# Kernel tuning notes

Measured on AMD Instinct MI355X. Metric: run time of the kernel, lower is better.

Reference implementation:

```python
import jax, jax.numpy as jnp
import numpy as np

B, N, C = 8, 4096, 512

def setup_inputs() -> dict:
    key = jax.random.key(0)
    k1, k2, k3, k4, k5, k6 = jax.random.split(key, 6)
    x = jax.random.normal(k1, (B, N, C), dtype=jnp.float32)
    adj = jax.random.uniform(k2, (B, C, C), dtype=jnp.float32)
    # params: stored [in, out] so y = x @ W + b (equivalent to torch Linear)
    s = 1.0 / np.sqrt(C)
    Wqkv = jax.random.uniform(k3, (C, 3 * C), dtype=jnp.float32, minval=-s, maxval=s)
    bqkv = jax.random.uniform(k4, (3 * C,), dtype=jnp.float32, minval=-s, maxval=s)
    Wo = jax.random.uniform(k5, (C, C), dtype=jnp.float32, minval=-s, maxval=s)
    bo = jax.random.uniform(k6, (C,), dtype=jnp.float32, minval=-s, maxval=s)
    return {"x": x, "adj": adj, "Wqkv": Wqkv, "bqkv": bqkv, "Wo": Wo, "bo": bo}

def reference(x, adj, Wqkv, bqkv, Wo, bo):
    # qkv projection + ReLU gating
    qkv = jnp.einsum('bnc,cd->bnd', x, Wqkv) + bqkv          # [B,N,3C]
    q, k, v = jnp.split(qkv, 3, axis=-1)                      # each [B,N,C]
    q, k, v = jax.nn.relu(q), jax.nn.relu(k), jax.nn.relu(v)
    dk = q.shape[-1]
    # channel-wise scores: q^T k over tokens -> [B,C,C]
    scores = jnp.einsum('bnc,bnd->bcd', q, k) / jnp.sqrt(jnp.float32(dk))
    attn = jax.nn.softmax(scores, axis=-1)
    attn = attn * adj                                         # post-softmax adjacency gate
    y = jnp.einsum('bnc,bcd->bnd', v, attn)                   # value.matmul(attention)
    return jnp.einsum('bnc,cd->bnd', y, Wo) + bo
```

## Files before the change

### kernel.cpp

```cpp
#include <hip/hip_runtime.h>

#define B_ 8
#define N_ 4096
#define C_ 512

typedef _Float16 f16;
typedef __attribute__((ext_vector_type(8))) _Float16 f16x8;
typedef __attribute__((ext_vector_type(4))) _Float16 f16x4;
typedef __attribute__((ext_vector_type(4))) float f32x4;

#define TILE_E (128 * 32)

#define GLL16(gsrc, ldst)                                                      \
  __builtin_amdgcn_global_load_lds(                                            \
      (const __attribute__((address_space(1))) void*)(gsrc),                   \
      (__attribute__((address_space(3))) void*)(ldst), 16, 0, 0)

__device__ __forceinline__ int xcd_remap(int bid, int nwg) {
  return (bid & 7) * (nwg >> 3) + (bid >> 3);
}

#define SBAR() asm volatile("s_barrier" ::: "memory")
#define SFENCE() __builtin_amdgcn_sched_barrier(0)

template <int LDA, int LDB, int NT>
__device__ __forceinline__ void mainloop8(const f16* __restrict__ Ag,
                                          const f16* __restrict__ Bg,
                                          f16* Als, f16* Bls,
                                          f32x4 (&acc)[8][4]) {
  const int tid = threadIdx.x;
  const int lane = tid & 63;
  const int wv = tid >> 6;
  const int wr = wv >> 2;
  const int wcq = wv & 3;

  const int kpart = ((lane >> 4) * 8) ^ ((lane & 4) << 2);
  const int abase = (lane & 15) * 64 + kpart;
  const int bbase = ((wcq & 1) * 64 + (lane & 15)) * 64 + kpart;

  int rowl[2], colb[2];
#pragma unroll
  for (int ld = 0; ld < 2; ++ld) {
    const int doff = (ld * 512 + tid) * 16;
    const int off2 = doff ^ (((doff >> 9) & 1) << 5);
    rowl[ld] = off2 >> 7;
    colb[ld] = off2 & 127;
  }

  const char* Agb = (const char*)Ag;
  const char* Bgb = (const char*)Bg;

  auto stage = [&](int t, int mat, int h) {
    if (t >= NT) return;
    const char* gb = mat ? Bgb : Agb;
    const int ldm2 = (mat ? LDB : LDA) * 2;
    f16* lsl = (mat ? Bls : Als) + ((t & 1) * 2 + h) * 8192 + wv * 512;
#pragma unroll
    for (int ld = 0; ld < 2; ++ld) {
      const char* src =
          gb + (size_t)(h * 128 + rowl[ld]) * ldm2 + (size_t)t * 128 + colb[ld];
      GLL16(src, lsl + ld * 4096);
    }
  };

  stage(0, 0, 0); stage(0, 0, 1); stage(0, 1, 0); stage(0, 1, 1);
  stage(1, 0, 0); stage(1, 0, 1); stage(1, 1, 0);
  asm volatile("s_waitcnt vmcnt(6)" ::: "memory");
  SBAR();
  SFENCE();

  for (int T = 0; T < NT; ++T) {
    const f16* Ab = Als + ((T & 1) * 2 + wr) * 8192;
    const f16* Bb = Bls + ((T & 1) * 2 + (wcq >> 1)) * 8192;
    stage(T + 1, 1, 1);
    f16x8 af[8][2], bf[4][2];
#pragma unroll
    for (int m = 0; m < 8; ++m)
#pragma unroll
      for (int s = 0; s < 2; ++s)
        af[m][s] = *(const f16x8*)(Ab + abase + m * 1024 + s * 32);
#pragma unroll
    for (int n = 0; n < 4; ++n)
#pragma unroll
      for (int s = 0; s < 2; ++s)
        bf[n][s] = *(const f16x8*)(Bb + bbase + n * 1024 + s * 32);
    asm volatile("" ::: "memory");
    SBAR();
    asm volatile("s_waitcnt lgkmcnt(0)" ::: "memory");
    SFENCE();
    __builtin_amdgcn_s_setprio(1);
#pragma unroll
    for (int m = 0; m < 4; ++m)
#pragma unroll
      for (int n = 0; n < 4; ++n)
        acc[m][n] = __builtin_amdgcn_mfma_f32_16x16x32_f16(af[m][0], bf[n][0],
                                                           acc[m][n], 0, 0, 0);
    __builtin_amdgcn_s_setprio(0);
    SBAR();
    SFENCE();
    stage(T + 2, 0, 0);
    SBAR();
    __builtin_amdgcn_s_setprio(1);
#pragma unroll
    for (int m = 4; m < 8; ++m)
#pragma unroll
      for (int n = 0; n < 4; ++n)
        acc[m][n] = __builtin_amdgcn_mfma_f32_16x16x32_f16(af[m][0], bf[n][0],
                                                           acc[m][n], 0, 0, 0);
    __builtin_amdgcn_s_setprio(0);
    SBAR();
    SFENCE();
    stage(T + 2, 0, 1);
    SBAR();
    __builtin_amdgcn_s_setprio(1);
#pragma unroll
    for (int m = 0; m < 4; ++m)
#pragma unroll
      for (int n = 0; n < 4; ++n)
        acc[m][n] = __builtin_amdgcn_mfma_f32_16x16x32_f16(af[m][1], bf[n][1],
                                                           acc[m][n], 0, 0, 0);
    __builtin_amdgcn_s_setprio(0);
    SBAR();
    SFENCE();
    stage(T + 2, 1, 0);
    if (T + 2 < NT) {
      asm volatile("s_waitcnt vmcnt(6)" ::: "memory");
    } else {
      asm volatile("s_waitcnt vmcnt(0)" ::: "memory");
    }
    SBAR();
    __builtin_amdgcn_s_setprio(1);
#pragma unroll
    for (int m = 4; m < 8; ++m)
#pragma unroll
      for (int n = 0; n < 4; ++n)
        acc[m][n] = __builtin_amdgcn_mfma_f32_16x16x32_f16(af[m][1], bf[n][1],
                                                           acc[m][n], 0, 0, 0);
    __builtin_amdgcn_s_setprio(0);
    SBAR();
    SFENCE();
  }
}

#define ZERO_ACC8(acc)                                                         \
  f32x4 acc[8][4];                                                             \
  _Pragma("unroll") for (int zi = 0; zi < 8; ++zi)                             \
      _Pragma("unroll") for (int zj = 0; zj < 4; ++zj) {                       \
    f32x4 z = {0.f, 0.f, 0.f, 0.f};                                            \
    acc[zi][zj] = z;                                                           \
  }

__device__ __forceinline__ void run_mainloop(const f16* __restrict__ Atile,
                                             const f16* __restrict__ Btile,
                                             int lda, int ldb, int nk,
                                             f16* As, f16* Bs,
                                             f32x4 (&acc)[4][4]) {
  const int tid = threadIdx.x;
  const int lane = tid & 63;
  const int wave = tid >> 6;
  const int wr = wave >> 1, wc = wave & 1;

  auto stage = [&](int buf, int kt) {
#pragma unroll
    for (int j = 0; j < 2; ++j) {
      const int idx = j * 256 + wave * 64 + lane;
      const int row = idx >> 2;
      const int kc = idx & 3;
      GLL16(Atile + (size_t)row * lda + kt * 32 + kc * 8,
            As + buf * TILE_E + (j * 256 + wave * 64) * 8);
      GLL16(Btile + (size_t)row * ldb + kt * 32 + kc * 8,
            Bs + buf * TILE_E + (j * 256 + wave * 64) * 8);
    }
  };

  stage(0, 0);
  __syncthreads();
  for (int kt = 0; kt < nk; ++kt) {
    const int buf = kt & 1;
    if (kt + 1 < nk) stage(buf ^ 1, kt + 1);
    const f16* aB = As + buf * TILE_E;
    const f16* bB = Bs + buf * TILE_E;
    f16x8 af[4], bf[4];
#pragma unroll
    for (int i = 0; i < 4; ++i)
      af[i] = *(const f16x8*)(aB + (wr * 64 + i * 16 + (lane & 15)) * 32 +
                              ((lane >> 4) * 8));
#pragma unroll
    for (int j = 0; j < 4; ++j)
      bf[j] = *(const f16x8*)(bB + (wc * 64 + j * 16 + (lane & 15)) * 32 +
                              ((lane >> 4) * 8));
#pragma unroll
    for (int i = 0; i < 4; ++i)
#pragma unroll
      for (int j = 0; j < 4; ++j)
        acc[i][j] =
            __builtin_amdgcn_mfma_f32_16x16x32_f16(af[i], bf[j], acc[i][j],
                                                   0, 0, 0);
    __syncthreads();
  }
}

#define ZERO_ACC(acc)                                                          \
  f32x4 acc[4][4];                                                             \
  _Pragma("unroll") for (int zi = 0; zi < 4; ++zi)                             \
      _Pragma("unroll") for (int zj = 0; zj < 4; ++zj) {                       \
    f32x4 z = {0.f, 0.f, 0.f, 0.f};                                            \
    acc[zi][zj] = z;                                                           \
  }

__global__ void __launch_bounds__(256) k_cvt_x(const float* __restrict__ in,
                                               f16* __restrict__ out) {
  const int i = blockIdx.x * 256 + threadIdx.x;
  float4 v = ((const float4*)in)[i];
  f16x4 h = {(f16)v.x, (f16)v.y, (f16)v.z, (f16)v.w};
  ((f16x4*)out)[i] = h;
}

__global__ void __launch_bounds__(256) k_transpose_w(const float* __restrict__ w,
                                                     f16* __restrict__ wt,
                                                     int cols) {
  const int idx = blockIdx.x * 256 + threadIdx.x;
  const int n = idx >> 9;
  const int c = idx & 511;
  wt[idx] = (f16)w[(size_t)c * cols + n];
}

__global__ void __launch_bounds__(512, 2)
    k_gemm_qkv(const f16* __restrict__ x16, const f16* __restrict__ wqkvt,
               const float* __restrict__ bqkv, f16* __restrict__ q_t,
               f16* __restrict__ k_t, f16* __restrict__ v16) {
  __shared__ alignas(16) f16 Als[4 * 8192];
  __shared__ alignas(16) f16 Bls[4 * 8192];
  const int l = xcd_remap(blockIdx.x, 768);
  const int bx = l % 6;
  const int rest = l / 6;
  const int by = rest & 15;
  const int b = rest >> 4;
  const f16* Ag = x16 + ((size_t)b * N_ + by * 256) * C_;
  const f16* Bg = wqkvt + (size_t)bx * 256 * C_;
  ZERO_ACC8(acc);
  mainloop8<C_, C_, C_ / 64>(Ag, Bg, Als, Bls, acc);

  const int lane = threadIdx.x & 63, wv = threadIdx.x >> 6;
  const int wr = wv >> 2, wcq = wv & 3;
  const int sec = bx >> 1;
  const int colloc = (bx & 1) * 256 + wcq * 64;
  const int rowbase = by * 256 + wr * 128;
#pragma unroll
  for (int n = 0; n < 4; ++n) {
    const int cch = colloc + n * 16 + (lane & 15);
    const float bias = bqkv[sec * 512 + cch];
#pragma unroll
    for (int m = 0; m < 8; ++m) {
      const int n0 = rowbase + m * 16 + ((lane >> 4) << 2);
      f32x4 a = acc[m][n];
      f16x4 h = {(f16)fmaxf(a[0] + bias, 0.f), (f16)fmaxf(a[1] + bias, 0.f),
                 (f16)fmaxf(a[2] + bias, 0.f), (f16)fmaxf(a[3] + bias, 0.f)};
      if (sec == 0) {
        *(f16x4*)(q_t + ((size_t)b * C_ + cch) * N_ + n0) = h;
      } else if (sec == 1) {
        *(f16x4*)(k_t + ((size_t)b * C_ + cch) * N_ + n0) = h;
      } else {
        f16* dst = v16 + ((size_t)b * N_ + n0) * C_ + cch;
        dst[0] = h[0];
        dst[C_] = h[1];
        dst[2 * C_] = h[2];
        dst[3 * C_] = h[3];
      }
    }
  }
}

__global__ void __launch_bounds__(512, 2)
    k_gemm_scores(const f16* __restrict__ q_t, const f16* __restrict__ k_t,
                  float* __restrict__ spart) {
  __shared__ alignas(16) f16 Als[4 * 8192];
  __shared__ alignas(16) f16 Bls[4 * 8192];
  const int l = xcd_remap(blockIdx.x, 128);
  const int bx = l & 1;
  const int by = (l >> 1) & 1;
  const int z = l >> 2;
  const int b = z >> 2, sp = z & 3;
  const f16* Ag = q_t + (size_t)b * C_ * N_ + (size_t)(by * 256) * N_ + sp * 1024;
  const f16* Bg = k_t + (size_t)b * C_ * N_ + (size_t)(bx * 256) * N_ + sp * 1024;
  ZERO_ACC8(acc);
  mainloop8<N_, N_, 1024 / 64>(Ag, Bg, Als, Bls, acc);

  const int lane = threadIdx.x & 63, wv = threadIdx.x >> 6;
  const int wr = wv >> 2, wcq = wv & 3;
  float* base = spart + (size_t)(sp * B_ + b) * C_ * C_;
#pragma unroll
  for (int n = 0; n < 4; ++n) {
    const int d = bx * 256 + wcq * 64 + n * 16 + (lane & 15);
#pragma unroll
    for (int m = 0; m < 8; ++m) {
      const int c0 = by * 256 + wr * 128 + m * 16 + ((lane >> 4) << 2);
#pragma unroll
      for (int r = 0; r < 4; ++r)
        base[(size_t)(c0 + r) * C_ + d] = acc[m][n][r];
    }
  }
}

__global__ void __launch_bounds__(256)
    k_softmax_gate(const float* __restrict__ spart,
                   const float* __restrict__ adj, f16* __restrict__ attn) {
  const int b = blockIdx.x >> 9, c = blockIdx.x & 511;
  const int tid = threadIdx.x;
  const size_t ro = ((size_t)b * C_ + c) * C_;
  float s0 = 0.f, s1 = 0.f;
#pragma unroll
  for (int sp = 0; sp < 4; ++sp) {
    const float* p = spart + (size_t)sp * B_ * C_ * C_ + ro;
    s0 += p[tid];
    s1 += p[tid + 256];
  }
  const float scale = 0.044194173824159216f;
  const float v0 = s0 * scale, v1 = s1 * scale;

  __shared__ float red[256];
  red[tid] = fmaxf(v0, v1);
  __syncthreads();
  for (int s = 128; s > 0; s >>= 1) {
    if (tid < s) red[tid] = fmaxf(red[tid], red[tid + s]);
    __syncthreads();
  }
  const float mx = red[0];
  __syncthreads();
  const float e0 = __expf(v0 - mx), e1 = __expf(v1 - mx);
  red[tid] = e0 + e1;
  __syncthreads();
  for (int s = 128; s > 0; s >>= 1) {
    if (tid < s) red[tid] += red[tid + s];
    __syncthreads();
  }
  const float inv = 1.0f / red[0];
  attn[ro + tid] = (f16)(e0 * inv * adj[ro + tid]);
  attn[ro + tid + 256] = (f16)(e1 * inv * adj[ro + tid + 256]);
}

__global__ void __launch_bounds__(256)
    k_gemm_m(const f16* __restrict__ attn, const f16* __restrict__ wot,
             f16* __restrict__ mt) {
  __shared__ alignas(16) f16 As[2 * TILE_E];
  __shared__ alignas(16) f16 Bs[2 * TILE_E];
  const int b = blockIdx.z;
  const f16* Atile = attn + (size_t)b * C_ * C_ + (size_t)blockIdx.y * 128 * C_;
  const f16* Btile = wot + (size_t)blockIdx.x * 128 * C_;
  ZERO_ACC(acc);
  run_mainloop(Atile, Btile, C_, C_, C_ / 32, As, Bs, acc);

  const int tid = threadIdx.x, lane = tid & 63, wave = tid >> 6;
  const int wr = wave >> 1, wc = wave & 1;
  f16* base = mt + (size_t)b * C_ * C_;
  const int colbase = blockIdx.x * 128 + wc * 64;
  const int rowbase = blockIdx.y * 128 + wr * 64;
#pragma unroll
  for (int j = 0; j < 4; ++j) {
    const int e = colbase + j * 16 + (lane & 15);
#pragma unroll
    for (int i = 0; i < 4; ++i) {
      const int c0 = rowbase + i * 16 + ((lane >> 4) << 2);
      f32x4 a = acc[i][j];
      f16x4 h = {(f16)a[0], (f16)a[1], (f16)a[2], (f16)a[3]};
      *(f16x4*)(base + (size_t)e * C_ + c0) = h;
    }
  }
}

__global__ void __launch_bounds__(512, 2)
    k_gemm_out(const f16* __restrict__ v16, const f16* __restrict__ mt,
               const float* __restrict__ bo, float* __restrict__ out) {
  __shared__ alignas(16) f16 Als[4 * 8192];
  __shared__ alignas(16) f16 Bls[4 * 8192];
  const int l = xcd_remap(blockIdx.x, 256);
  const int bx = l & 1;
  const int by = (l >> 1) & 15;
  const int b = l >> 5;
  const f16* Ag = v16 + ((size_t)b * N_ + by * 256) * C_;
  const f16* Bg = mt + (size_t)b * C_ * C_ + (size_t)(bx * 256) * C_;
  ZERO_ACC8(acc);
  mainloop8<C_, C_, C_ / 64>(Ag, Bg, Als, Bls, acc);

  const int lane = threadIdx.x & 63, wv = threadIdx.x >> 6;
  const int wr = wv >> 2, wcq = wv & 3;
  float* base = out + (size_t)b * N_ * C_;
#pragma unroll
  for (int n = 0; n < 4; ++n) {
    const int e = bx * 256 + wcq * 64 + n * 16 + (lane & 15);
    const float bias = bo[e];
#pragma unroll
    for (int m = 0; m < 8; ++m) {
      const int n0 = by * 256 + wr * 128 + m * 16 + ((lane >> 4) << 2);
#pragma unroll
      for (int r = 0; r < 4; ++r)
        base[(size_t)(n0 + r) * C_ + e] = acc[m][n][r] + bias;
    }
  }
}

extern "C" void kernel_launch(void* const* d_in, const int* in_sizes, int n_in,
                              void* d_out, int out_size, void* d_ws,
                              size_t ws_size, hipStream_t stream) {
  const float* x = (const float*)d_in[0];
  const float* adj = (const float*)d_in[1];
  const float* Wqkv = (const float*)d_in[2];
  const float* bqkv = (const float*)d_in[3];
  const float* Wo = (const float*)d_in[4];
  const float* bo = (const float*)d_in[5];
  float* out = (float*)d_out;

  char* ws = (char*)d_ws;
  size_t off = 0;
  auto carve = [&](size_t bytes) -> char* {
    char* p = ws + off;
    off += (bytes + 255) & ~(size_t)255;
    return p;
  };
  f16* x16 = (f16*)carve((size_t)B_ * N_ * C_ * 2);
  f16* wqkvt = (f16*)carve((size_t)3 * C_ * C_ * 2);
  f16* wot = (f16*)carve((size_t)C_ * C_ * 2);
  f16* q_t = (f16*)carve((size_t)B_ * C_ * N_ * 2);
  f16* k_t = (f16*)carve((size_t)B_ * C_ * N_ * 2);
  f16* v16 = (f16*)carve((size_t)B_ * N_ * C_ * 2);
  float* spart = (float*)x16;
  f16* attn16 = k_t;
  f16* mt16 = q_t;

  k_cvt_x<<<(B_ * N_ * C_ / 4) / 256, 256, 0, stream>>>(x, x16);
  k_transpose_w<<<(C_ * 3 * C_) / 256, 256, 0, stream>>>(Wqkv, wqkvt, 3 * C_);
  k_transpose_w<<<(C_ * C_) / 256, 256, 0, stream>>>(Wo, wot, C_);
  k_gemm_qkv<<<768, 512, 0, stream>>>(x16, wqkvt, bqkv, q_t, k_t, v16);
  k_gemm_scores<<<128, 512, 0, stream>>>(q_t, k_t, spart);
  k_softmax_gate<<<B_ * C_, 256, 0, stream>>>(spart, adj, attn16);
  k_gemm_m<<<dim3(4, 4, B_), 256, 0, stream>>>(attn16, wot, mt16);
  k_gemm_out<<<256, 512, 0, stream>>>(v16, mt16, bo, out);
}
```

Before: 198.6 us.

## Persistent multi-tile QKV GEMM, wider split-K scores with fp16 partials

The GEMM mainloop becomes generic over source lambdas and an epilogue callback, so one block can sweep several output tiles while keeping the LDS double-buffer pipeline running across tile boundaries. The QKV projection now launches 256 blocks, each covering three 256-column tiles and reusing its x row panel, instead of 768 single-tile blocks. The scores GEMM switches to 8-way split-K with 256 blocks and stores fp16 partials instead of fp32, halving partial-sum traffic and filling more CUs. The risk is the fp16 rounding of partial scores before softmax, and the QKV kernel now uses a third as many blocks.

```diff
diff --git a/kernel.cpp b/kernel.cpp
--- a/kernel.cpp
+++ b/kernel.cpp
@@ -23,11 +23,10 @@
 #define SBAR() asm volatile("s_barrier" ::: "memory")
 #define SFENCE() __builtin_amdgcn_sched_barrier(0)
 
-template <int LDA, int LDB, int NT>
-__device__ __forceinline__ void mainloop8(const f16* __restrict__ Ag,
-                                          const f16* __restrict__ Bg,
-                                          f16* Als, f16* Bls,
-                                          f32x4 (&acc)[8][4]) {
+template <int LDA2, int LDB2, int NTT, int SUBNT, typename ASrc, typename BSrc,
+          typename Epi>
+__device__ __forceinline__ void mainloop8p(ASrc asrc, BSrc bsrc, f16* Als,
+                                           f16* Bls, Epi epi) {
   const int tid = threadIdx.x;
   const int lane = tid & 63;
   const int wv = tid >> 6;
@@ -47,20 +46,24 @@
     colb[ld] = off2 & 127;
   }
 
-  const char* Agb = (const char*)Ag;
-  const char* Bgb = (const char*)Bg;
+  f32x4 acc[8][4];
+#pragma unroll
+  for (int zi = 0; zi < 8; ++zi)
+#pragma unroll
+    for (int zj = 0; zj < 4; ++zj) {
+      f32x4 z = {0.f, 0.f, 0.f, 0.f};
+      acc[zi][zj] = z;
+    }
 
   auto stage = [&](int t, int mat, int h) {
-    if (t >= NT) return;
-    const char* gb = mat ? Bgb : Agb;
-    const int ldm2 = (mat ? LDB : LDA) * 2;
+    if (t >= NTT) return;
+    const char* s0 = mat ? bsrc(t) : asrc(t);
+    const int LD2 = mat ? LDB2 : LDA2;
     f16* lsl = (mat ? Bls : Als) + ((t & 1) * 2 + h) * 8192 + wv * 512;
 #pragma unroll
-    for (int ld = 0; ld < 2; ++ld) {
-      const char* src =
-          gb + (size_t)(h * 128 + rowl[ld]) * ldm2 + (size_t)t * 128 + colb[ld];
-      GLL16(src, lsl + ld * 4096);
-    }
+    for (int ld = 0; ld < 2; ++ld)
+      GLL16(s0 + (size_t)(h * 128 + rowl[ld]) * LD2 + colb[ld],
+            lsl + ld * 4096);
   };
 
   stage(0, 0, 0); stage(0, 0, 1); stage(0, 1, 0); stage(0, 1, 1);
@@ -69,86 +72,91 @@
   SBAR();
   SFENCE();
 
-  for (int T = 0; T < NT; ++T) {
-    const f16* Ab = Als + ((T & 1) * 2 + wr) * 8192;
-    const f16* Bb = Bls + ((T & 1) * 2 + (wcq >> 1)) * 8192;
-    stage(T + 1, 1, 1);
-    f16x8 af[8][2], bf[4][2];
-#pragma unroll
-    for (int m = 0; m < 8; ++m)
-#pragma unroll
-      for (int s = 0; s < 2; ++s)
-        af[m][s] = *(const f16x8*)(Ab + abase + m * 1024 + s * 32);
-#pragma unroll
-    for (int n = 0; n < 4; ++n)
-#pragma unroll
-      for (int s = 0; s < 2; ++s)
-        bf[n][s] = *(const f16x8*)(Bb + bbase + n * 1024 + s * 32);
-    asm volatile("" ::: "memory");
-    SBAR();
-    asm volatile("s_waitcnt lgkmcnt(0)" ::: "memory");
-    SFENCE();
-    __builtin_amdgcn_s_setprio(1);
-#pragma unroll
-    for (int m = 0; m < 4; ++m)
+#pragma unroll 1
+  for (int g = 0; g < NTT / SUBNT; ++g) {
+#pragma unroll
+    for (int Ti = 0; Ti < SUBNT; ++Ti) {
+      const int T = g * SUBNT + Ti;
+      const f16* Ab = Als + ((Ti & 1) * 2 + wr) * 8192;
+      const f16* Bb = Bls + ((Ti & 1) * 2 + (wcq >> 1)) * 8192;
+      stage(T + 1, 1, 1);
+      f16x8 af[8][2], bf[4][2];
+#pragma unroll
+      for (int m = 0; m < 8; ++m)
+#pragma unroll
+        for (int s = 0; s < 2; ++s)
+          af[m][s] = *(const f16x8*)(Ab + abase + m * 1024 + s * 32);
 #pragma unroll
       for (int n = 0; n < 4; ++n)
-        acc[m][n] = __builtin_amdgcn_mfma_f32_16x16x32_f16(af[m][0], bf[n][0],
-                                                           acc[m][n], 0, 0, 0);
-    __builtin_amdgcn_s_setprio(0);
-    SBAR();
-    SFENCE();
-    stage(T + 2, 0, 0);
-    SBAR();
-    __builtin_amdgcn_s_setprio(1);
-#pragma unroll
-    for (int m = 4; m < 8; ++m)
-#pragma unroll
-      for (int n = 0; n < 4; ++n)
-        acc[m][n] = __builtin_amdgcn_mfma_f32_16x16x32_f16(af[m][0], bf[n][0],
-                                                           acc[m][n], 0, 0, 0);
-    __builtin_amdgcn_s_setprio(0);
-    SBAR();
-    SFENCE();
-    stage(T + 2, 0, 1);
-    SBAR();
-    __builtin_amdgcn_s_setprio(1);
-#pragma unroll
-    for (int m = 0; m < 4; ++m)
-#pragma unroll
-      for (int n = 0; n < 4; ++n)
-        acc[m][n] = __builtin_amdgcn_mfma_f32_16x16x32_f16(af[m][1], bf[n][1],
-                                                           acc[m][n], 0, 0, 0);
-    __builtin_amdgcn_s_setprio(0);
-    SBAR();
-    SFENCE();
-    stage(T + 2, 1, 0);
-    if (T + 2 < NT) {
-      asm volatile("s_waitcnt vmcnt(6)" ::: "memory");
-    } else {
-      asm volatile("s_waitcnt vmcnt(0)" ::: "memory");
-    }
-    SBAR();
-    __builtin_amdgcn_s_setprio(1);
-#pragma unroll
-    for (int m = 4; m < 8; ++m)
-#pragma unroll
-      for (int n = 0; n < 4; ++n)
-        acc[m][n] = __builtin_amdgcn_mfma_f32_16x16x32_f16(af[m][1], bf[n][1],
-                                                           acc[m][n], 0, 0, 0);
-    __builtin_amdgcn_s_setprio(0);
-    SBAR();
-    SFENCE();
-  }
-}
-
-#define ZERO_ACC8(acc)                                                         \
-  f32x4 acc[8][4];                                                             \
-  _Pragma("unroll") for (int zi = 0; zi < 8; ++zi)                             \
-      _Pragma("unroll") for (int zj = 0; zj < 4; ++zj) {                       \
-    f32x4 z = {0.f, 0.f, 0.f, 0.f};                                            \
-    acc[zi][zj] = z;                                                           \
-  }
+#pragma unroll
+        for (int s = 0; s < 2; ++s)
+          bf[n][s] = *(const f16x8*)(Bb + bbase + n * 1024 + s * 32);
+      asm volatile("" ::: "memory");
+      SBAR();
+      asm volatile("s_waitcnt lgkmcnt(0)" ::: "memory");
+      SFENCE();
+      __builtin_amdgcn_s_setprio(1);
+#pragma unroll
+      for (int m = 0; m < 4; ++m)
+#pragma unroll
+        for (int n = 0; n < 4; ++n)
+          acc[m][n] = __builtin_amdgcn_mfma_f32_16x16x32_f16(
+              af[m][0], bf[n][0], acc[m][n], 0, 0, 0);
+      __builtin_amdgcn_s_setprio(0);
+      SBAR();
+      SFENCE();
+      stage(T + 2, 0, 0);
+      SBAR();
+      __builtin_amdgcn_s_setprio(1);
+#pragma unroll
+      for (int m = 4; m < 8; ++m)
+#pragma unroll
+        for (int n = 0; n < 4; ++n)
+          acc[m][n] = __builtin_amdgcn_mfma_f32_16x16x32_f16(
+              af[m][0], bf[n][0], acc[m][n], 0, 0, 0);
+      __builtin_amdgcn_s_setprio(0);
+      SBAR();
+      SFENCE();
+      stage(T + 2, 0, 1);
+      SBAR();
+      __builtin_amdgcn_s_setprio(1);
+#pragma unroll
+      for (int m = 0; m < 4; ++m)
+#pragma unroll
+        for (int n = 0; n < 4; ++n)
+          acc[m][n] = __builtin_amdgcn_mfma_f32_16x16x32_f16(
+              af[m][1], bf[n][1], acc[m][n], 0, 0, 0);
+      __builtin_amdgcn_s_setprio(0);
+      SBAR();
+      SFENCE();
+      stage(T + 2, 1, 0);
+      if (T + 2 < NTT) {
+        asm volatile("s_waitcnt vmcnt(6)" ::: "memory");
+      } else {
+        asm volatile("s_waitcnt vmcnt(0)" ::: "memory");
+      }
+      SBAR();
+      __builtin_amdgcn_s_setprio(1);
+#pragma unroll
+      for (int m = 4; m < 8; ++m)
+#pragma unroll
+        for (int n = 0; n < 4; ++n)
+          acc[m][n] = __builtin_amdgcn_mfma_f32_16x16x32_f16(
+              af[m][1], bf[n][1], acc[m][n], 0, 0, 0);
+      __builtin_amdgcn_s_setprio(0);
+      SBAR();
+      SFENCE();
+    }
+    epi(g, acc);
+#pragma unroll
+    for (int zi = 0; zi < 8; ++zi)
+#pragma unroll
+      for (int zj = 0; zj < 4; ++zj) {
+        f32x4 z = {0.f, 0.f, 0.f, 0.f};
+        acc[zi][zj] = z;
+      }
+  }
+}
 
 __device__ __forceinline__ void run_mainloop(const f16* __restrict__ Atile,
                                              const f16* __restrict__ Btile,
@@ -231,89 +239,99 @@
                f16* __restrict__ k_t, f16* __restrict__ v16) {
   __shared__ alignas(16) f16 Als[4 * 8192];
   __shared__ alignas(16) f16 Bls[4 * 8192];
-  const int l = xcd_remap(blockIdx.x, 768);
-  const int bx = l % 6;
-  const int rest = l / 6;
-  const int by = rest & 15;
-  const int b = rest >> 4;
-  const f16* Ag = x16 + ((size_t)b * N_ + by * 256) * C_;
-  const f16* Bg = wqkvt + (size_t)bx * 256 * C_;
-  ZERO_ACC8(acc);
-  mainloop8<C_, C_, C_ / 64>(Ag, Bg, Als, Bls, acc);
-
+  const int l = xcd_remap(blockIdx.x, 256);
+  const int cg = l & 1;
+  const int by = (l >> 1) & 15;
+  const int b = l >> 5;
+  const char* Agb = (const char*)(x16 + ((size_t)b * N_ + by * 256) * C_);
+  const char* Bgb = (const char*)(wqkvt + (size_t)cg * 3 * 256 * C_);
   const int lane = threadIdx.x & 63, wv = threadIdx.x >> 6;
   const int wr = wv >> 2, wcq = wv & 3;
-  const int sec = bx >> 1;
-  const int colloc = (bx & 1) * 256 + wcq * 64;
-  const int rowbase = by * 256 + wr * 128;
-#pragma unroll
-  for (int n = 0; n < 4; ++n) {
-    const int cch = colloc + n * 16 + (lane & 15);
-    const float bias = bqkv[sec * 512 + cch];
-#pragma unroll
-    for (int m = 0; m < 8; ++m) {
-      const int n0 = rowbase + m * 16 + ((lane >> 4) << 2);
-      f32x4 a = acc[m][n];
-      f16x4 h = {(f16)fmaxf(a[0] + bias, 0.f), (f16)fmaxf(a[1] + bias, 0.f),
-                 (f16)fmaxf(a[2] + bias, 0.f), (f16)fmaxf(a[3] + bias, 0.f)};
-      if (sec == 0) {
-        *(f16x4*)(q_t + ((size_t)b * C_ + cch) * N_ + n0) = h;
-      } else if (sec == 1) {
-        *(f16x4*)(k_t + ((size_t)b * C_ + cch) * N_ + n0) = h;
-      } else {
-        f16* dst = v16 + ((size_t)b * N_ + n0) * C_ + cch;
-        dst[0] = h[0];
-        dst[C_] = h[1];
-        dst[2 * C_] = h[2];
-        dst[3 * C_] = h[3];
+
+  auto asrc = [&](int t) { return Agb + (t & 7) * 128; };
+  auto bsrc = [&](int t) {
+    return Bgb + (size_t)(t >> 3) * (256 * C_ * 2) + (t & 7) * 128;
+  };
+  auto epi = [&](int g, f32x4 (&acc)[8][4]) {
+    const int ct = cg * 3 + g;
+    const int sec = ct >> 1;
+    const int colloc = (ct & 1) * 256 + wcq * 64;
+    const int rowbase = by * 256 + wr * 128;
+#pragma unroll
+    for (int n = 0; n < 4; ++n) {
+      const int cch = colloc + n * 16 + (lane & 15);
+      const float bias = bqkv[sec * 512 + cch];
+#pragma unroll
+      for (int m = 0; m < 8; ++m) {
+        const int n0 = rowbase + m * 16 + ((lane >> 4) << 2);
+        f32x4 a = acc[m][n];
+        f16x4 h = {(f16)fmaxf(a[0] + bias, 0.f), (f16)fmaxf(a[1] + bias, 0.f),
+                   (f16)fmaxf(a[2] + bias, 0.f), (f16)fmaxf(a[3] + bias, 0.f)};
+        if (sec == 0) {
+          *(f16x4*)(q_t + ((size_t)b * C_ + cch) * N_ + n0) = h;
+        } else if (sec == 1) {
+          *(f16x4*)(k_t + ((size_t)b * C_ + cch) * N_ + n0) = h;
+        } else {
+          f16* dst = v16 + ((size_t)b * N_ + n0) * C_ + cch;
+          dst[0] = h[0];
+          dst[C_] = h[1];
+          dst[2 * C_] = h[2];
+          dst[3 * C_] = h[3];
+        }
       }
     }
-  }
+  };
+  mainloop8p<C_ * 2, C_ * 2, 24, 8>(asrc, bsrc, Als, Bls, epi);
 }
 
 __global__ void __launch_bounds__(512, 2)
     k_gemm_scores(const f16* __restrict__ q_t, const f16* __restrict__ k_t,
-                  float* __restrict__ spart) {
+                  f16* __restrict__ spart) {
   __shared__ alignas(16) f16 Als[4 * 8192];
   __shared__ alignas(16) f16 Bls[4 * 8192];
-  const int l = xcd_remap(blockIdx.x, 128);
+  const int l = xcd_remap(blockIdx.x, 256);
   const int bx = l & 1;
   const int by = (l >> 1) & 1;
   const int z = l >> 2;
-  const int b = z >> 2, sp = z & 3;
-  const f16* Ag = q_t + (size_t)b * C_ * N_ + (size_t)(by * 256) * N_ + sp * 1024;
-  const f16* Bg = k_t + (size_t)b * C_ * N_ + (size_t)(bx * 256) * N_ + sp * 1024;
-  ZERO_ACC8(acc);
-  mainloop8<N_, N_, 1024 / 64>(Ag, Bg, Als, Bls, acc);
-
+  const int b = z >> 3, sp = z & 7;
+  const char* Agb = (const char*)(q_t + (size_t)b * C_ * N_ +
+                                  (size_t)(by * 256) * N_ + sp * 512);
+  const char* Bgb = (const char*)(k_t + (size_t)b * C_ * N_ +
+                                  (size_t)(bx * 256) * N_ + sp * 512);
   const int lane = threadIdx.x & 63, wv = threadIdx.x >> 6;
   const int wr = wv >> 2, wcq = wv & 3;
-  float* base = spart + (size_t)(sp * B_ + b) * C_ * C_;
-#pragma unroll
-  for (int n = 0; n < 4; ++n) {
-    const int d = bx * 256 + wcq * 64 + n * 16 + (lane & 15);
-#pragma unroll
-    for (int m = 0; m < 8; ++m) {
-      const int c0 = by * 256 + wr * 128 + m * 16 + ((lane >> 4) << 2);
-#pragma unroll
-      for (int r = 0; r < 4; ++r)
-        base[(size_t)(c0 + r) * C_ + d] = acc[m][n][r];
-    }
-  }
+
+  auto asrc = [&](int t) { return Agb + t * 128; };
+  auto bsrc = [&](int t) { return Bgb + t * 128; };
+  f16* base = spart + (size_t)(sp * B_ + b) * C_ * C_;
+  auto epi = [&](int g, f32x4 (&acc)[8][4]) {
+#pragma unroll
+    for (int n = 0; n < 4; ++n) {
+      const int d = bx * 256 + wcq * 64 + n * 16 + (lane & 15);
+#pragma unroll
+      for (int m = 0; m < 8; ++m) {
+        const int c0 = by * 256 + wr * 128 + m * 16 + ((lane >> 4) << 2);
+#pragma unroll
+        for (int r = 0; r < 4; ++r)
+          base[(size_t)(c0 + r) * C_ + d] = (f16)acc[m][n][r];
+      }
+    }
+  };
+  mainloop8p<N_ * 2, N_ * 2, 8, 8>(asrc, bsrc, Als, Bls, epi);
 }
 
 __global__ void __launch_bounds__(256)
-    k_softmax_gate(const float* __restrict__ spart,
+    k_softmax_gate(const f16* __restrict__ spart,
                    const float* __restrict__ adj, f16* __restrict__ attn) {
   const int b = blockIdx.x >> 9, c = blockIdx.x & 511;
   const int tid = threadIdx.x;
   const size_t ro = ((size_t)b * C_ + c) * C_;
   float s0 = 0.f, s1 = 0.f;
 #pragma unroll
-  for (int sp = 0; sp < 4; ++sp) {
-    const float* p = spart + (size_t)sp * B_ * C_ * C_ + ro;
-    s0 += p[tid];
-    s1 += p[tid + 256];
+  for (int sp = 0; sp < 8; ++sp) {
+    const f16* p = spart + (size_t)sp * B_ * C_ * C_ + ro;
+    s0 += (float)p[tid];
+    s1 += (float)p[tid + 256];
   }
   const float scale = 0.044194173824159216f;
   const float v0 = s0 * scale, v1 = s1 * scale;
@@ -377,26 +395,30 @@
   const int bx = l & 1;
   const int by = (l >> 1) & 15;
   const int b = l >> 5;
-  const f16* Ag = v16 + ((size_t)b * N_ + by * 256) * C_;
-  const f16* Bg = mt + (size_t)b * C_ * C_ + (size_t)(bx * 256) * C_;
-  ZERO_ACC8(acc);
-  mainloop8<C_, C_, C_ / 64>(Ag, Bg, Als, Bls, acc);
-
+  const char* Agb = (const char*)(v16 + ((size_t)b * N_ + by * 256) * C_);
+  const char* Bgb = (const char*)(mt + (size_t)b * C_ * C_ +
+                                  (size_t)(bx * 256) * C_);
   const int lane = threadIdx.x & 63, wv = threadIdx.x >> 6;
   const int wr = wv >> 2, wcq = wv & 3;
+
+  auto asrc = [&](int t) { return Agb + t * 128; };
+  auto bsrc = [&](int t) { return Bgb + t * 128; };
   float* base = out + (size_t)b * N_ * C_;
-#pragma unroll
-  for (int n = 0; n < 4; ++n) {
-    const int e = bx * 256 + wcq * 64 + n * 16 + (lane & 15);
-    const float bias = bo[e];
-#pragma unroll
-    for (int m = 0; m < 8; ++m) {
-      const int n0 = by * 256 + wr * 128 + m * 16 + ((lane >> 4) << 2);
-#pragma unroll
-      for (int r = 0; r < 4; ++r)
-        base[(size_t)(n0 + r) * C_ + e] = acc[m][n][r] + bias;
-    }
-  }
+  auto epi = [&](int g, f32x4 (&acc)[8][4]) {
+#pragma unroll
+    for (int n = 0; n < 4; ++n) {
+      const int e = bx * 256 + wcq * 64 + n * 16 + (lane & 15);
+      const float bias = bo[e];
+#pragma unroll
+      for (int m = 0; m < 8; ++m) {
+        const int n0 = by * 256 + wr * 128 + m * 16 + ((lane >> 4) << 2);
+#pragma unroll
+        for (int r = 0; r < 4; ++r)
+          base[(size_t)(n0 + r) * C_ + e] = acc[m][n][r] + bias;
+      }
+    }
+  };
+  mainloop8p<C_ * 2, C_ * 2, 8, 8>(asrc, bsrc, Als, Bls, epi);
 }
 
 extern "C" void kernel_launch(void* const* d_in, const int* in_sizes, int n_in,
@@ -423,15 +445,15 @@
   f16* q_t = (f16*)carve((size_t)B_ * C_ * N_ * 2);
   f16* k_t = (f16*)carve((size_t)B_ * C_ * N_ * 2);
   f16* v16 = (f16*)carve((size_t)B_ * N_ * C_ * 2);
-  float* spart = (float*)x16;
+  f16* spart = x16;
   f16* attn16 = k_t;
   f16* mt16 = q_t;
 
   k_cvt_x<<<(B_ * N_ * C_ / 4) / 256, 256, 0, stream>>>(x, x16);
   k_transpose_w<<<(C_ * 3 * C_) / 256, 256, 0, stream>>>(Wqkv, wqkvt, 3 * C_);
   k_transpose_w<<<(C_ * C_) / 256, 256, 0, stream>>>(Wo, wot, C_);
-  k_gemm_qkv<<<768, 512, 0, stream>>>(x16, wqkvt, bqkv, q_t, k_t, v16);
-  k_gemm_scores<<<128, 512, 0, stream>>>(q_t, k_t, spart);
+  k_gemm_qkv<<<256, 512, 0, stream>>>(x16, wqkvt, bqkv, q_t, k_t, v16);
+  k_gemm_scores<<<256, 512, 0, stream>>>(q_t, k_t, spart);
   k_softmax_gate<<<B_ * C_, 256, 0, stream>>>(spart, adj, attn16);
   k_gemm_m<<<dim3(4, 4, B_), 256, 0, stream>>>(attn16, wot, mt16);
   k_gemm_out<<<256, 512, 0, stream>>>(v16, mt16, bo, out);
```

Result: slower. 264.3 us (+33.1%).

## Swizzle LDS layout, split lgkm waits, double split-K for scores with fp16 partials

Applied to the files above, without the earlier changes.

The shared GEMM mainloop gets a new XOR swizzle on the LDS layout (row&7 based) to reduce bank conflicts, and its fragment loads are reordered so the first MFMA batch waits only for part of the LDS reads (lgkmcnt(4)), with a full wait before the second k-half. The scores GEMM now splits the token reduction 8 ways instead of 4, launching 256 blocks instead of 128 to fill more CUs, and stores partial sums as fp16 rather than fp32 to halve the partial traffic. Storing partial scores in fp16 adds rounding error before the softmax.

```diff
diff --git a/kernel.cpp b/kernel.cpp
--- a/kernel.cpp
+++ b/kernel.cpp
@@ -23,9 +23,9 @@
 #define SBAR() asm volatile("s_barrier" ::: "memory")
 #define SFENCE() __builtin_amdgcn_sched_barrier(0)
 
-template <int LDA, int LDB, int NT>
-__device__ __forceinline__ void mainloop8(const f16* __restrict__ Ag,
-                                          const f16* __restrict__ Bg,
+template <int LDA2, int LDB2, int NT>
+__device__ __forceinline__ void mainloop8(const char* __restrict__ Agb,
+                                          const char* __restrict__ Bgb,
                                           f16* Als, f16* Bls,
                                           f32x4 (&acc)[8][4]) {
   const int tid = threadIdx.x;
@@ -34,33 +34,30 @@
   const int wr = wv >> 2;
   const int wcq = wv & 3;
 
-  const int kpart = ((lane >> 4) * 8) ^ ((lane & 4) << 2);
-  const int abase = (lane & 15) * 64 + kpart;
-  const int bbase = ((wcq & 1) * 64 + (lane & 15)) * 64 + kpart;
+  const int r15 = lane & 15;
+  const int kc8 = (lane >> 4) << 3;
+  const int swz = (r15 & 7) << 3;
+  const int aoff = r15 * 64;
+  const int boff = ((wcq & 1) * 64 + r15) * 64;
 
   int rowl[2], colb[2];
 #pragma unroll
   for (int ld = 0; ld < 2; ++ld) {
     const int doff = (ld * 512 + tid) * 16;
-    const int off2 = doff ^ (((doff >> 9) & 1) << 5);
-    rowl[ld] = off2 >> 7;
-    colb[ld] = off2 & 127;
-  }
-
-  const char* Agb = (const char*)Ag;
-  const char* Bgb = (const char*)Bg;
+    rowl[ld] = doff >> 7;
+    colb[ld] = (doff & 127) ^ ((rowl[ld] & 7) << 4);
+  }
 
   auto stage = [&](int t, int mat, int h) {
     if (t >= NT) return;
     const char* gb = mat ? Bgb : Agb;
-    const int ldm2 = (mat ? LDB : LDA) * 2;
+    const int LD2 = mat ? LDB2 : LDA2;
     f16* lsl = (mat ? Bls : Als) + ((t & 1) * 2 + h) * 8192 + wv * 512;
 #pragma unroll
-    for (int ld = 0; ld < 2; ++ld) {
-      const char* src =
-          gb + (size_t)(h * 128 + rowl[ld]) * ldm2 + (size_t)t * 128 + colb[ld];
-      GLL16(src, lsl + ld * 4096);
-    }
+    for (int ld = 0; ld < 2; ++ld)
+      GLL16(gb + (size_t)(h * 128 + rowl[ld]) * LD2 + (size_t)t * 128 +
+                colb[ld],
+            lsl + ld * 4096);
   };
 
   stage(0, 0, 0); stage(0, 0, 1); stage(0, 1, 0); stage(0, 1, 1);
@@ -78,15 +75,19 @@
     for (int m = 0; m < 8; ++m)
 #pragma unroll
       for (int s = 0; s < 2; ++s)
-        af[m][s] = *(const f16x8*)(Ab + abase + m * 1024 + s * 32);
+        af[m][s] =
+            *(const f16x8*)(Ab + aoff + m * 1024 + ((kc8 + s * 32) ^ swz));
+    SFENCE();
 #pragma unroll
     for (int n = 0; n < 4; ++n)
-#pragma unroll
-      for (int s = 0; s < 2; ++s)
-        bf[n][s] = *(const f16x8*)(Bb + bbase + n * 1024 + s * 32);
-    asm volatile("" ::: "memory");
-    SBAR();
-    asm volatile("s_waitcnt lgkmcnt(0)" ::: "memory");
+      bf[n][0] = *(const f16x8*)(Bb + boff + n * 1024 + (kc8 ^ swz));
+    SFENCE();
+#pragma unroll
+    for (int n = 0; n < 4; ++n)
+      bf[n][1] = *(const f16x8*)(Bb + boff + n * 1024 + ((kc8 + 32) ^ swz));
+    SFENCE();
+    SBAR();
+    asm volatile("s_waitcnt lgkmcnt(4)" ::: "memory");
     SFENCE();
     __builtin_amdgcn_s_setprio(1);
 #pragma unroll
@@ -112,6 +113,8 @@
     SFENCE();
     stage(T + 2, 0, 1);
     SBAR();
+    asm volatile("s_waitcnt lgkmcnt(0)" ::: "memory");
+    SFENCE();
     __builtin_amdgcn_s_setprio(1);
 #pragma unroll
     for (int m = 0; m < 4; ++m)
@@ -236,10 +239,10 @@
   const int rest = l / 6;
   const int by = rest & 15;
   const int b = rest >> 4;
-  const f16* Ag = x16 + ((size_t)b * N_ + by * 256) * C_;
-  const f16* Bg = wqkvt + (size_t)bx * 256 * C_;
+  const char* Agb = (const char*)(x16 + ((size_t)b * N_ + by * 256) * C_);
+  const char* Bgb = (const char*)(wqkvt + (size_t)bx * 256 * C_);
   ZERO_ACC8(acc);
-  mainloop8<C_, C_, C_ / 64>(Ag, Bg, Als, Bls, acc);
+  mainloop8<C_ * 2, C_ * 2, C_ / 64>(Agb, Bgb, Als, Bls, acc);
 
   const int lane = threadIdx.x & 63, wv = threadIdx.x >> 6;
   const int wr = wv >> 2, wcq = wv & 3;
@@ -273,22 +276,24 @@
 
 __global__ void __launch_bounds__(512, 2)
     k_gemm_scores(const f16* __restrict__ q_t, const f16* __restrict__ k_t,
-                  float* __restrict__ spart) {
+                  f16* __restrict__ spart) {
   __shared__ alignas(16) f16 Als[4 * 8192];
   __shared__ alignas(16) f16 Bls[4 * 8192];
-  const int l = xcd_remap(blockIdx.x, 128);
+  const int l = xcd_remap(blockIdx.x, 256);
   const int bx = l & 1;
   const int by = (l >> 1) & 1;
   const int z = l >> 2;
-  const int b = z >> 2, sp = z & 3;
-  const f16* Ag = q_t + (size_t)b * C_ * N_ + (size_t)(by * 256) * N_ + sp * 1024;
-  const f16* Bg = k_t + (size_t)b * C_ * N_ + (size_t)(bx * 256) * N_ + sp * 1024;
+  const int b = z >> 3, sp = z & 7;
+  const char* Agb = (const char*)(q_t + (size_t)b * C_ * N_ +
+                                  (size_t)(by * 256) * N_ + sp * 512);
+  const char* Bgb = (const char*)(k_t + (size_t)b * C_ * N_ +
+                                  (size_t)(bx * 256) * N_ + sp * 512);
   ZERO_ACC8(acc);
-  mainloop8<N_, N_, 1024 / 64>(Ag, Bg, Als, Bls, acc);
+  mainloop8<N_ * 2, N_ * 2, 8>(Agb, Bgb, Als, Bls, acc);
 
   const int lane = threadIdx.x & 63, wv = threadIdx.x >> 6;
   const int wr = wv >> 2, wcq = wv & 3;
-  float* base = spart + (size_t)(sp * B_ + b) * C_ * C_;
+  f16* base = spart + (size_t)(sp * B_ + b) * C_ * C_;
 #pragma unroll
   for (int n = 0; n < 4; ++n) {
     const int d = bx * 256 + wcq * 64 + n * 16 + (lane & 15);
@@ -297,23 +302,23 @@
       const int c0 = by * 256 + wr * 128 + m * 16 + ((lane >> 4) << 2);
 #pragma unroll
       for (int r = 0; r < 4; ++r)
-        base[(size_t)(c0 + r) * C_ + d] = acc[m][n][r];
+        base[(size_t)(c0 + r) * C_ + d] = (f16)acc[m][n][r];
     }
   }
 }
 
 __global__ void __launch_bounds__(256)
-    k_softmax_gate(const float* __restrict__ spart,
+    k_softmax_gate(const f16* __restrict__ spart,
                    const float* __restrict__ adj, f16* __restrict__ attn) {
   const int b = blockIdx.x >> 9, c = blockIdx.x & 511;
   const int tid = threadIdx.x;
   const size_t ro = ((size_t)b * C_ + c) * C_;
   float s0 = 0.f, s1 = 0.f;
 #pragma unroll
-  for (int sp = 0; sp < 4; ++sp) {
-    const float* p = spart + (size_t)sp * B_ * C_ * C_ + ro;
-    s0 += p[tid];
-    s1 += p[tid + 256];
+  for (int sp = 0; sp < 8; ++sp) {
+    const f16* p = spart + (size_t)sp * B_ * C_ * C_ + ro;
+    s0 += (float)p[tid];
+    s1 += (float)p[tid + 256];
   }
   const float scale = 0.044194173824159216f;
   const float v0 = s0 * scale, v1 = s1 * scale;
@@ -377,10 +382,11 @@
   const int bx = l & 1;
   const int by = (l >> 1) & 15;
   const int b = l >> 5;
-  const f16* Ag = v16 + ((size_t)b * N_ + by * 256) * C_;
-  const f16* Bg = mt + (size_t)b * C_ * C_ + (size_t)(bx * 256) * C_;
+  const char* Agb = (const char*)(v16 + ((size_t)b * N_ + by * 256) * C_);
+  const char* Bgb = (const char*)(mt + (size_t)b * C_ * C_ +
+                                  (size_t)(bx * 256) * C_);
   ZERO_ACC8(acc);
-  mainloop8<C_, C_, C_ / 64>(Ag, Bg, Als, Bls, acc);
+  mainloop8<C_ * 2, C_ * 2, 8>(Agb, Bgb, Als, Bls, acc);
 
   const int lane = threadIdx.x & 63, wv = threadIdx.x >> 6;
   const int wr = wv >> 2, wcq = wv & 3;
@@ -423,7 +429,7 @@
   f16* q_t = (f16*)carve((size_t)B_ * C_ * N_ * 2);
   f16* k_t = (f16*)carve((size_t)B_ * C_ * N_ * 2);
   f16* v16 = (f16*)carve((size_t)B_ * N_ * C_ * 2);
-  float* spart = (float*)x16;
+  f16* spart = x16;
   f16* attn16 = k_t;
   f16* mt16 = q_t;
 
@@ -431,7 +437,7 @@
   k_transpose_w<<<(C_ * 3 * C_) / 256, 256, 0, stream>>>(Wqkv, wqkvt, 3 * C_);
   k_transpose_w<<<(C_ * C_) / 256, 256, 0, stream>>>(Wo, wot, C_);
   k_gemm_qkv<<<768, 512, 0, stream>>>(x16, wqkvt, bqkv, q_t, k_t, v16);
-  k_gemm_scores<<<128, 512, 0, stream>>>(q_t, k_t, spart);
+  k_gemm_scores<<<256, 512, 0, stream>>>(q_t, k_t, spart);
   k_softmax_gate<<<B_ * C_, 256, 0, stream>>>(spart, adj, attn16);
   k_gemm_m<<<dim3(4, 4, B_), 256, 0, stream>>>(attn16, wot, mt16);
   k_gemm_out<<<256, 512, 0, stream>>>(v16, mt16, bo, out);
```

Measured after the change: 179.9 us. -9.4%, faster.
